# Kernel optimization log

Hardware: AMD Instinct MI355X
Metric: run time of the kernel (lower is better)

## Reference

```python
import jax, jax.numpy as jnp
import numpy as np

DIM = 768
HEADS = 8
HEAD_DIM = DIM // HEADS
K_TOP = 10
NUM_ANSWERS = 128000
BATCH = 1024
LN_EPS = 1e-5
NORM_EPS = 1e-12


def setup_inputs() -> dict:
    key = jax.random.key(0)
    ks = jax.random.split(key, 16)
    s = 0.02  # weight init scale
    return {
        "visual_feat": jax.random.normal(ks[0], (BATCH, DIM), jnp.float32),
        "text_feat": jax.random.normal(ks[1], (BATCH, DIM), jnp.float32),
        "candidate_mask": (jax.random.uniform(ks[2], (BATCH, NUM_ANSWERS), jnp.float32) > 0.5).astype(jnp.float32),
        "answer_embeddings": jax.random.normal(ks[3], (NUM_ANSWERS, DIM), jnp.float32),
        # MultiheadAttention params (torch layout: y = x @ W.T + b)
        "wq": jax.random.normal(ks[4], (DIM, DIM), jnp.float32) * s,
        "bq": jnp.zeros((DIM,), jnp.float32),
        "wk": jax.random.normal(ks[5], (DIM, DIM), jnp.float32) * s,
        "bk": jnp.zeros((DIM,), jnp.float32),
        "wv": jax.random.normal(ks[6], (DIM, DIM), jnp.float32) * s,
        "bv": jnp.zeros((DIM,), jnp.float32),
        "wo": jax.random.normal(ks[7], (DIM, DIM), jnp.float32) * s,
        "bo": jnp.zeros((DIM,), jnp.float32),
        # fusion_proj: Linear(2*dim -> dim) + LayerNorm(dim)
        "fusion_w": jax.random.normal(ks[8], (DIM, 2 * DIM), jnp.float32) * s,
        "fusion_b": jnp.zeros((DIM,), jnp.float32),
        "ln_g": jnp.ones((DIM,), jnp.float32),
        "ln_b": jnp.zeros((DIM,), jnp.float32),
        # similarity_proj: Linear(dim -> dim)
        "sim_w": jax.random.normal(ks[9], (DIM, DIM), jnp.float32) * s,
        "sim_b": jnp.zeros((DIM,), jnp.float32),
    }


def _l2norm(x):
    # F.normalize: x / clamp_min(||x||, eps)
    n = jnp.sqrt(jnp.sum(x * x, axis=-1, keepdims=True))
    return x / jnp.maximum(n, NORM_EPS)


def _forward(visual_feat, text_feat, candidate_mask, answer_embeddings,
             wq, bq, wk, bk, wv, bv, wo, bo,
             fusion_w, fusion_b, ln_g, ln_b, sim_w, sim_b):
    B = visual_feat.shape[0]
    # Multihead attention with q=text (len 1), k=v=visual (len 1).
    q = text_feat @ wq.T + bq            # [B, D]
    k = visual_feat @ wk.T + bk          # [B, D]
    v = visual_feat @ wv.T + bv          # [B, D]
    qh = q.reshape(B, HEADS, HEAD_DIM)
    kh = k.reshape(B, HEADS, HEAD_DIM)
    vh = v.reshape(B, HEADS, HEAD_DIM)
    scores = jnp.sum(qh * kh, axis=-1) / jnp.sqrt(jnp.float32(HEAD_DIM))  # [B, H]
    # softmax over the single key position -> identically 1
    attn_w = jax.nn.softmax(scores[..., None], axis=-1)                   # [B, H, 1]
    attended = (attn_w * vh).reshape(B, DIM) @ wo.T + bo                  # [B, D]
    # fusion_proj: Linear -> LayerNorm -> GELU (dropout is identity in eval)
    fused_in = jnp.concatenate([visual_feat, attended], axis=-1)          # [B, 2D]
    h = fused_in @ fusion_w.T + fusion_b                                  # [B, D]
    mu = jnp.mean(h, axis=-1, keepdims=True)
    var = jnp.mean((h - mu) ** 2, axis=-1, keepdims=True)
    h = (h - mu) / jnp.sqrt(var + LN_EPS) * ln_g + ln_b
    fused = jax.nn.gelu(h, approximate=False)
    fused_proj = fused @ sim_w.T + sim_b                                  # [B, D]
    # normalize + similarity GEMM + mask + top-k + gather
    similarity = _l2norm(fused_proj) @ _l2norm(answer_embeddings).T       # [B, A]
    similarity = similarity * candidate_mask
    topk_scores, topk_indices = jax.lax.top_k(similarity, K_TOP)          # [B, K]
    topk_embeddings = answer_embeddings[topk_indices]                     # [B, K, D]
    return topk_scores, topk_indices, topk_embeddings


def reference(visual_feat, text_feat, candidate_mask, answer_embeddings,
              wq, bq, wk, bk, wv, bv, wo, bo,
              fusion_w, fusion_b, ln_g, ln_b, sim_w, sim_b):
    return _forward(visual_feat, text_feat, candidate_mask, answer_embeddings,
                    wq, bq, wk, bk, wv, bv, wo, bo,
                    fusion_w, fusion_b, ln_g, ln_b, sim_w, sim_b)
```

## Files before the change

kernel.cpp:

```cpp
#include <hip/hip_runtime.h>
#include <math.h>

#define DIM    768
#define BATCH  1024
#define NANS   128000
#define NT128  1000
#define NWORDS 4000

typedef short  bf16x8 __attribute__((ext_vector_type(8)));
typedef float  f32x4  __attribute__((ext_vector_type(4)));
typedef unsigned long long u64;

__device__ __forceinline__ short f2bf(float x)
{
    unsigned u = __builtin_bit_cast(unsigned, x);
    u += 0x7fffu + ((u >> 16) & 1u);
    return (short)(u >> 16);
}

__device__ __forceinline__ void gload16(const void* g, void* l)
{
    __builtin_amdgcn_global_load_lds(
        (const __attribute__((address_space(1))) void*)g,
        (__attribute__((address_space(3))) void*)l, 16, 0, 0);
}

__device__ __forceinline__ unsigned f2sort(float s)
{
    unsigned u = __builtin_bit_cast(unsigned, s);
    return u ^ ((unsigned)((int)u >> 31) | 0x80000000u);
}

__device__ __forceinline__ unsigned umaxu(unsigned a, unsigned b) { return a > b ? a : b; }
__device__ __forceinline__ unsigned uminu(unsigned a, unsigned b) { return a < b ? a : b; }

struct Top10k { unsigned k0,k1,k2,k3,k4,k5,k6,k7,k8,k9; };
__device__ __forceinline__ void t10k_init(Top10k& t)
{ t.k0=t.k1=t.k2=t.k3=t.k4=t.k5=t.k6=t.k7=t.k8=t.k9=0u; }
__device__ __forceinline__ void t10k_ins(Top10k& t, unsigned v)
{
#define TS(K) { unsigned mx = umaxu(v, t.K); v = uminu(v, t.K); t.K = mx; }
    TS(k0) TS(k1) TS(k2) TS(k3) TS(k4) TS(k5) TS(k6) TS(k7) TS(k8) TS(k9)
#undef TS
}

struct Top16u { u64 k0,k1,k2,k3,k4,k5,k6,k7,k8,k9,k10,k11,k12,k13,k14,k15; };
__device__ __forceinline__ void t16u_init(Top16u& t)
{
    t.k0=t.k1=t.k2=t.k3=t.k4=t.k5=t.k6=t.k7=0ull;
    t.k8=t.k9=t.k10=t.k11=t.k12=t.k13=t.k14=t.k15=0ull;
}
__device__ __forceinline__ void t16u_ins(Top16u& t, u64 v)
{
#define TS(K) { bool g = v > t.K; u64 mx = g ? v : t.K; v = g ? t.K : v; t.K = mx; }
    TS(k0)  TS(k1)  TS(k2)  TS(k3)  TS(k4)  TS(k5)  TS(k6)  TS(k7)
    TS(k8)  TS(k9)  TS(k10) TS(k11) TS(k12) TS(k13) TS(k14) TS(k15)
#undef TS
}

__global__ __launch_bounds__(256, 2) void gemm_bias_k(
    const float* __restrict__ A, int lda,
    const float* __restrict__ W,
    const float* __restrict__ bias,
    float* __restrict__ C, int ldc, int K)
{
    __shared__ float as[32][68];
    __shared__ float bs[32][68];
    int m0 = blockIdx.x * 64, n0 = blockIdx.y * 64;
    int tid = threadIdx.x;
    int tm = tid & 15, tn = tid >> 4;
    int sr = tid >> 3, skq = tid & 7;
    float acc[4][4] = {};
    for (int k0 = 0; k0 < K; k0 += 32) {
        __syncthreads();
        #pragma unroll
        for (int p = 0; p < 2; ++p) {
            int r = sr + 32 * p;
            float4 av = *(const float4*)&A[(size_t)(m0 + r) * lda + k0 + skq * 4];
            as[skq*4+0][r] = av.x; as[skq*4+1][r] = av.y;
            as[skq*4+2][r] = av.z; as[skq*4+3][r] = av.w;
            float4 wv = *(const float4*)&W[(size_t)(n0 + r) * K + k0 + skq * 4];
            bs[skq*4+0][r] = wv.x; bs[skq*4+1][r] = wv.y;
            bs[skq*4+2][r] = wv.z; bs[skq*4+3][r] = wv.w;
        }
        __syncthreads();
        #pragma unroll 8
        for (int k = 0; k < 32; ++k) {
            float a4[4], b4[4];
            *(float4*)a4 = *(const float4*)&as[k][tm*4];
            *(float4*)b4 = *(const float4*)&bs[k][tn*4];
            #pragma unroll
            for (int i = 0; i < 4; ++i)
                #pragma unroll
                for (int j = 0; j < 4; ++j)
                    acc[i][j] = fmaf(a4[i], b4[j], acc[i][j]);
        }
    }
    float4 bv4 = *(const float4*)&bias[n0 + tn*4];
    #pragma unroll
    for (int i = 0; i < 4; ++i) {
        float4 c4;
        c4.x = acc[i][0] + bv4.x; c4.y = acc[i][1] + bv4.y;
        c4.z = acc[i][2] + bv4.z; c4.w = acc[i][3] + bv4.w;
        *(float4*)&C[(size_t)(m0 + tm*4 + i) * ldc + n0 + tn*4] = c4;
    }
}

__global__ void copy_visual_k(const float* __restrict__ src, float* __restrict__ dst)
{
    int idx = blockIdx.x * 256 + threadIdx.x;
    const int total = BATCH * (DIM / 4);
    for (; idx < total; idx += 512 * 256) {
        int b = idx / (DIM / 4), c = idx % (DIM / 4);
        ((float4*)dst)[(size_t)b * (1536 / 4) + c] = ((const float4*)src)[idx];
    }
}

__device__ __forceinline__ float block_sum(float v, float* red)
{
    #pragma unroll
    for (int o = 32; o; o >>= 1) v += __shfl_down(v, o);
    if ((threadIdx.x & 63) == 0) red[threadIdx.x >> 6] = v;
    __syncthreads();
    float r = red[0] + red[1] + red[2] + red[3];
    __syncthreads();
    return r;
}

__global__ __launch_bounds__(256) void ln_gelu_k(float* __restrict__ H,
        const float* __restrict__ g, const float* __restrict__ b)
{
    __shared__ float red[4];
    int row = blockIdx.x, tid = threadIdx.x;
    float* hr = H + (size_t)row * DIM;
    float v0 = hr[tid], v1 = hr[tid + 256], v2 = hr[tid + 512];
    float mu = block_sum(v0 + v1 + v2, red) * (1.0f / 768.0f);
    float d0 = v0 - mu, d1 = v1 - mu, d2 = v2 - mu;
    float var = block_sum(d0*d0 + d1*d1 + d2*d2, red) * (1.0f / 768.0f);
    float rinv = 1.0f / sqrtf(var + 1e-5f);
    #pragma unroll
    for (int q = 0; q < 3; ++q) {
        int d = tid + 256 * q;
        float dd = (q == 0 ? d0 : (q == 1 ? d1 : d2));
        float y = dd * rinv * g[d] + b[d];
        hr[d] = 0.5f * y * (1.0f + erff(y * 0.70710678118654752f));
    }
}

__global__ __launch_bounds__(256) void l2norm_bf_k(float* __restrict__ P,
        short* __restrict__ Pb)
{
    __shared__ float red[4];
    int row = blockIdx.x, tid = threadIdx.x;
    float* pr = P + (size_t)row * DIM;
    short* pb = Pb + (size_t)row * DIM;
    float v0 = pr[tid], v1 = pr[tid + 256], v2 = pr[tid + 512];
    float ss = block_sum(v0*v0 + v1*v1 + v2*v2, red);
    float inv = 1.0f / fmaxf(sqrtf(ss), 1e-12f);
    v0 *= inv; v1 *= inv; v2 *= inv;
    pr[tid] = v0; pr[tid + 256] = v1; pr[tid + 512] = v2;
    pb[tid] = f2bf(v0); pb[tid + 256] = f2bf(v1); pb[tid + 512] = f2bf(v2);
}

__global__ __launch_bounds__(256) void prep_ans_k(
    const float* __restrict__ ANS, int row0, int nrows,
    double* __restrict__ inv64, short* __restrict__ AB)
{
    int r = blockIdx.x * 4 + (threadIdx.x >> 6);
    if (r >= nrows) return;
    int row = row0 + r;
    int lane = threadIdx.x & 63;
    const float4* a4 = (const float4*)(ANS + (size_t)row * DIM);
    float4 x0 = a4[lane], x1 = a4[lane + 64], x2 = a4[lane + 128];
    double ss = (double)x0.x*x0.x + (double)x0.y*x0.y + (double)x0.z*x0.z + (double)x0.w*x0.w
              + (double)x1.x*x1.x + (double)x1.y*x1.y + (double)x1.z*x1.z + (double)x1.w*x1.w
              + (double)x2.x*x2.x + (double)x2.y*x2.y + (double)x2.z*x2.z + (double)x2.w*x2.w;
    #pragma unroll
    for (int o = 32; o; o >>= 1) ss += __shfl_xor(ss, o);
    double inv = 1.0 / fmax(sqrt(ss), 1e-12);
    if (lane == 0) inv64[row] = inv;
    float invf = (float)inv;
    short* ob = AB + (size_t)r * DIM;
    ushort4 o0, o1, o2;
    o0.x = (unsigned short)f2bf(x0.x*invf); o0.y = (unsigned short)f2bf(x0.y*invf);
    o0.z = (unsigned short)f2bf(x0.z*invf); o0.w = (unsigned short)f2bf(x0.w*invf);
    o1.x = (unsigned short)f2bf(x1.x*invf); o1.y = (unsigned short)f2bf(x1.y*invf);
    o1.z = (unsigned short)f2bf(x1.z*invf); o1.w = (unsigned short)f2bf(x1.w*invf);
    o2.x = (unsigned short)f2bf(x2.x*invf); o2.y = (unsigned short)f2bf(x2.y*invf);
    o2.z = (unsigned short)f2bf(x2.z*invf); o2.w = (unsigned short)f2bf(x2.w*invf);
    *(ushort4*)&ob[lane * 4]           = o0;
    *(ushort4*)&ob[(lane + 64) * 4]    = o1;
    *(ushort4*)&ob[(lane + 128) * 4]   = o2;
}

__global__ __launch_bounds__(256, 4) void prep_maskT_k(
    const float* __restrict__ mask, unsigned* __restrict__ bitsT)
{
    int r = blockIdx.x * 256 + threadIdx.x;
    int w0 = blockIdx.y * 40;
    const float* mr = mask + (size_t)r * NANS;
    for (int w = w0; w < w0 + 40; ++w) {
        const float4* p = (const float4*)(mr + w * 32);
        unsigned b = 0;
        #pragma unroll
        for (int q = 0; q < 8; ++q) {
            float4 v = p[q];
            b |= ((unsigned)(v.x != 0.f)) << (q*4+0);
            b |= ((unsigned)(v.y != 0.f)) << (q*4+1);
            b |= ((unsigned)(v.z != 0.f)) << (q*4+2);
            b |= ((unsigned)(v.w != 0.f)) << (q*4+3);
        }
        bitsT[(size_t)w * BATCH + r] = b;
    }
}

__global__ __launch_bounds__(256, 2) void gemmsel_k(
    const short* __restrict__ Pb,
    const short* __restrict__ AB,
    const unsigned* __restrict__ bitsT,
    unsigned* __restrict__ ck,
    int t128_0, int nt128)
{
    __shared__ __align__(16) char smem[33792];
    float* scl = (float*)smem;

    int bid = blockIdx.x;
    int v = (bid & 7) * nt128 + (bid >> 3);
    int at = v >> 3, bt = v & 7;
    int gt = t128_0 + at;
    int a0l = at * 128, b0 = bt * 128;

    int tid = threadIdx.x;
    int lane = tid & 63, wid = tid >> 6;
    int wm = wid & 1, wn = wid >> 1;
    int lr = lane & 15, lg = lane >> 4;

    const char* gA0 = (const char*)(AB + (size_t)(a0l + (tid >> 2)) * DIM + (tid & 3) * 8);
    const char* gA1 = (const char*)(AB + (size_t)(a0l + 64 + (tid >> 2)) * DIM + (tid & 3) * 8);
    const char* gB0 = (const char*)(Pb + (size_t)(b0 + (tid >> 2)) * DIM + (tid & 3) * 8);
    const char* gB1 = (const char*)(Pb + (size_t)(b0 + 64 + (tid >> 2)) * DIM + (tid & 3) * 8);

    f32x4 acc[4][4];
    #pragma unroll
    for (int i = 0; i < 4; ++i)
        #pragma unroll
        for (int j = 0; j < 4; ++j)
            acc[i][j] = (f32x4){0.f, 0.f, 0.f, 0.f};

    {
        char* la = smem + tid * 16;
        gload16(gA0, la);
        gload16(gA1, la + 4096);
        gload16(gB0, la + 16384);
        gload16(gB1, la + 20480);
    }
    __syncthreads();

    int buf = 0;
    for (int kt = 0; kt < 24; ++kt) {
        if (kt < 23) {
            int kb = (kt + 1) * 64;
            char* la = smem + (buf ^ 1) * 8192 + tid * 16;
            gload16(gA0 + kb, la);
            gload16(gA1 + kb, la + 4096);
            gload16(gB0 + kb, la + 16384);
            gload16(gB1 + kb, la + 20480);
        }
        const short* a_sh = (const short*)(smem + buf * 8192);
        const short* b_sh = (const short*)(smem + 16384 + buf * 8192);
        bf16x8 af[4], bg[4];
        #pragma unroll
        for (int mt = 0; mt < 4; ++mt)
            af[mt] = *(const bf16x8*)(a_sh + (wm*64 + mt*16 + lr) * 32 + lg*8);
        #pragma unroll
        for (int nt = 0; nt < 4; ++nt)
            bg[nt] = *(const bf16x8*)(b_sh + (wn*64 + nt*16 + lr) * 32 + lg*8);
        #pragma unroll
        for (int mt = 0; mt < 4; ++mt)
            #pragma unroll
            for (int nt = 0; nt < 4; ++nt)
                acc[mt][nt] = __builtin_amdgcn_mfma_f32_16x16x32_bf16(
                    af[mt], bg[nt], acc[mt][nt], 0, 0, 0);
        __syncthreads();
        buf ^= 1;
    }

    Top10k tp;
    t10k_init(tp);
    int col = tid >> 1, qt = tid & 1;
    int qoff = qt * 32;

    for (int c = 0; c < 2; ++c) {
        __syncthreads();
        if (wm == c) {
            #pragma unroll
            for (int nt = 0; nt < 4; ++nt) {
                int lcol = wn * 64 + nt * 16 + lr;
                #pragma unroll
                for (int mt = 0; mt < 4; ++mt) {
                    int lrow = mt * 16 + lg * 4;
                    scl[(lrow + 0) * 132 + lcol] = acc[mt][nt][0];
                    scl[(lrow + 1) * 132 + lcol] = acc[mt][nt][1];
                    scl[(lrow + 2) * 132 + lcol] = acc[mt][nt][2];
                    scl[(lrow + 3) * 132 + lcol] = acc[mt][nt][3];
                }
            }
        }
        __syncthreads();
        unsigned wv = bitsT[(size_t)(gt * 4 + c * 2 + qt) * BATCH + b0 + col];
        unsigned lobc = (unsigned)(127 - c * 64 - qoff);
        #pragma unroll
        for (int i = 0; i < 32; ++i) {
            float sc = scl[(qoff + i) * 132 + col];
            sc = ((wv >> i) & 1u) ? sc : 0.0f;
            unsigned key = (f2sort(sc) & 0xFFFFFF80u) | (lobc - (unsigned)i);
            t10k_ins(tp, key);
        }
    }

    unsigned q0 = __shfl_xor(tp.k0, 1), q1 = __shfl_xor(tp.k1, 1);
    unsigned q2 = __shfl_xor(tp.k2, 1), q3 = __shfl_xor(tp.k3, 1);
    unsigned q4 = __shfl_xor(tp.k4, 1), q5 = __shfl_xor(tp.k5, 1);
    unsigned q6 = __shfl_xor(tp.k6, 1), q7 = __shfl_xor(tp.k7, 1);
    unsigned q8 = __shfl_xor(tp.k8, 1), q9 = __shfl_xor(tp.k9, 1);
    if (qt == 0) {
        unsigned* dst = ck + (size_t)(b0 + col) * (NT128 * 10) + (size_t)gt * 10;
        dst[0] = umaxu(tp.k0, q9);
        dst[1] = umaxu(tp.k1, q8);
        dst[2] = umaxu(tp.k2, q7);
        dst[3] = umaxu(tp.k3, q6);
        dst[4] = umaxu(tp.k4, q5);
        dst[5] = umaxu(tp.k5, q4);
        dst[6] = umaxu(tp.k6, q3);
        dst[7] = umaxu(tp.k7, q2);
        dst[8] = umaxu(tp.k8, q1);
        dst[9] = umaxu(tp.k9, q0);
    }
}

__global__ __launch_bounds__(256) void merge_rescore5_k(
    const unsigned* __restrict__ ck,
    const float* __restrict__ P, const float* __restrict__ ANS,
    const double* __restrict__ invn64, const float* __restrict__ mask,
    float* __restrict__ out)
{
    __shared__ u64    lk[4096];
    __shared__ u64    rrk[4];
    __shared__ int    rrp[4];
    __shared__ int    topi_s[16];
    __shared__ double tops_s[16];
    __shared__ int    fin_s[10];
    int row = blockIdx.x, tid = threadIdx.x;

    Top16u t;
    t16u_init(t);
    const unsigned* ckr = ck + (size_t)row * (NT128 * 10);
    for (int j = tid; j < NT128 * 10; j += 256)
        t16u_ins(t, ((u64)ckr[j] << 32) | (unsigned)j);
    {
        int o = tid * 16;
        lk[o+0]=t.k0;  lk[o+1]=t.k1;  lk[o+2]=t.k2;  lk[o+3]=t.k3;
        lk[o+4]=t.k4;  lk[o+5]=t.k5;  lk[o+6]=t.k6;  lk[o+7]=t.k7;
        lk[o+8]=t.k8;  lk[o+9]=t.k9;  lk[o+10]=t.k10; lk[o+11]=t.k11;
        lk[o+12]=t.k12; lk[o+13]=t.k13; lk[o+14]=t.k14; lk[o+15]=t.k15;
    }
    __syncthreads();

    for (int it = 0; it < 16; ++it) {
        u64 bk = 0; int bp = -1;
        for (int j = tid; j < 4096; j += 256) {
            u64 k = lk[j];
            if (k > bk) { bk = k; bp = j; }
        }
        #pragma unroll
        for (int o = 32; o; o >>= 1) {
            u64 ok = __shfl_down(bk, o);
            int op = __shfl_down(bp, o);
            if (ok > bk) { bk = ok; bp = op; }
        }
        if ((tid & 63) == 0) { rrk[tid >> 6] = bk; rrp[tid >> 6] = bp; }
        __syncthreads();
        if (tid == 0) {
            for (int w = 1; w < 4; ++w)
                if (rrk[w] > bk) { bk = rrk[w]; bp = rrp[w]; }
            unsigned key = (unsigned)(bk >> 32);
            int pos = (int)(bk & 0xffffffffull);
            topi_s[it] = (pos / 10) * 128 + 127 - (int)(key & 0x7Fu);
            lk[bp] = 0;
        }
        __syncthreads();
    }

    int c = tid >> 4, part = tid & 15;
    int aidx = topi_s[c];
    const float4* p4 = (const float4*)(P + (size_t)row * DIM);
    const float4* a4 = (const float4*)(ANS + (size_t)aidx * DIM);
    double sum = 0.0;
    #pragma unroll
    for (int i = 0; i < 12; ++i) {
        float4 pv = p4[part * 12 + i];
        float4 av = a4[part * 12 + i];
        sum += (double)pv.x * av.x + (double)pv.y * av.y
             + (double)pv.z * av.z + (double)pv.w * av.w;
    }
    #pragma unroll
    for (int o = 8; o; o >>= 1) sum += __shfl_down(sum, o, 16);
    if (part == 0) {
        float m = mask[(size_t)row * NANS + aidx];
        tops_s[c] = sum * invn64[aidx] * (double)m;
    }
    __syncthreads();

    if (tid == 0) {
        unsigned used = 0;
        for (int k = 0; k < 10; ++k) {
            int bj = -1;
            for (int j = 0; j < 16; ++j) {
                if (used & (1u << j)) continue;
                if (bj < 0 || tops_s[j] > tops_s[bj] ||
                    (tops_s[j] == tops_s[bj] && topi_s[j] < topi_s[bj])) bj = j;
            }
            used |= 1u << bj;
            out[(size_t)row * 10 + k] = (float)tops_s[bj];
            out[10240 + (size_t)row * 10 + k] = (float)topi_s[bj];
            fin_s[k] = topi_s[bj];
        }
    }
    __syncthreads();

    for (int k = 0; k < 10; ++k) {
        int id = fin_s[k];
        const float* arow = ANS + (size_t)id * DIM;
        float* orow = out + 20480 + ((size_t)(row * 10 + k)) * DIM;
        for (int d = tid; d < DIM; d += 256) orow[d] = arow[d];
    }
}

extern "C" void kernel_launch(void* const* d_in, const int* in_sizes, int n_in,
                              void* d_out, int out_size, void* d_ws, size_t ws_size,
                              hipStream_t stream)
{
    (void)in_sizes; (void)n_in; (void)out_size;
    const float* visual = (const float*)d_in[0];
    const float* mask   = (const float*)d_in[2];
    const float* ans    = (const float*)d_in[3];
    const float* wv = (const float*)d_in[8];
    const float* bv = (const float*)d_in[9];
    const float* wo = (const float*)d_in[10];
    const float* bo = (const float*)d_in[11];
    const float* fw = (const float*)d_in[12];
    const float* fb = (const float*)d_in[13];
    const float* lg = (const float*)d_in[14];
    const float* lb = (const float*)d_in[15];
    const float* sw = (const float*)d_in[16];
    const float* sb = (const float*)d_in[17];
    float* out = (float*)d_out;

    char* w = (char*)d_ws;
    float*    P      = (float*)w;    w += (size_t)BATCH * DIM * 4;
    short*    Pb     = (short*)w;    w += (size_t)BATCH * DIM * 2;
    double*   invn64 = (double*)w;   w += (size_t)NANS * 8;
    unsigned* ck     = (unsigned*)w; w += (size_t)BATCH * NT128 * 10 * 4;
    unsigned* bitsT  = (unsigned*)w; w += (size_t)NWORDS * BATCH * 4;
    char*     tail   = w;
    float*    fused_in = (float*)tail;
    float*    v        = fused_in + (size_t)BATCH * 1536;
    float*    h        = v + (size_t)BATCH * DIM;
    short*    AB       = (short*)tail;

    size_t ab_t = (size_t)128 * DIM * 2;
    size_t used = (size_t)(tail - (char*)d_ws);
    size_t avail = (ws_size > used) ? (ws_size - used) : ab_t;
    int CT = (int)(avail / ab_t);
    if (CT < 1) CT = 1;
    if (CT > NT128) CT = NT128;
    int nch = (NT128 + CT - 1) / CT;

    copy_visual_k<<<512, 256, 0, stream>>>(visual, fused_in);
    gemm_bias_k<<<dim3(16, 12), 256, 0, stream>>>(visual, DIM, wv, bv, v, DIM, DIM);
    gemm_bias_k<<<dim3(16, 12), 256, 0, stream>>>(v, DIM, wo, bo, fused_in + DIM, 1536, DIM);
    gemm_bias_k<<<dim3(16, 12), 256, 0, stream>>>(fused_in, 1536, fw, fb, h, DIM, 1536);
    ln_gelu_k<<<BATCH, 256, 0, stream>>>(h, lg, lb);
    gemm_bias_k<<<dim3(16, 12), 256, 0, stream>>>(h, DIM, sw, sb, P, DIM, DIM);
    l2norm_bf_k<<<BATCH, 256, 0, stream>>>(P, Pb);
    prep_maskT_k<<<dim3(4, 100), 256, 0, stream>>>(mask, bitsT);

    for (int ch = 0; ch < nch; ++ch) {
        int t0 = ch * CT;
        int n = NT128 - t0; if (n > CT) n = CT;
        int nrows = n * 128;
        prep_ans_k<<<(nrows + 3) / 4, 256, 0, stream>>>(ans, t0 * 128, nrows,
                                                        invn64, AB);
        gemmsel_k<<<n * 8, 256, 0, stream>>>(Pb, AB, bitsT, ck, t0, n);
    }

    merge_rescore5_k<<<BATCH, 256, 0, stream>>>(ck, P, ans, invn64, mask, out);
}
```

Measured before the change: 965.8 us.

## Split fusion GEMM to drop concat copy, retile mask prep, transpose score staging

The concat copy of visual features is removed. The fusion projection is computed as two K=768 GEMMs, the second one accumulating into the output, with a weight-stride parameter added to gemm_bias_k. The mask bit-packing kernel launches twice as many blocks, each handling half as many words, to raise parallelism on the large mask read. The score staging in gemmsel is transposed to a column-major layout so each thread writes and reads float4 vectors instead of scalars. Together these aim to cut copies, LDS instruction count and mask-prep latency, at the cost of one extra GEMM launch and a read-modify-write pass over the fusion output.

```diff
diff --git a/kernel.cpp b/kernel.cpp
--- a/kernel.cpp
+++ b/kernel.cpp
@@ -60,9 +60,9 @@
 
 __global__ __launch_bounds__(256, 2) void gemm_bias_k(
     const float* __restrict__ A, int lda,
-    const float* __restrict__ W,
+    const float* __restrict__ W, int wstride,
     const float* __restrict__ bias,
-    float* __restrict__ C, int ldc, int K)
+    float* __restrict__ C, int ldc, int K, int accum)
 {
     __shared__ float as[32][68];
     __shared__ float bs[32][68];
@@ -79,7 +79,7 @@
             float4 av = *(const float4*)&A[(size_t)(m0 + r) * lda + k0 + skq * 4];
             as[skq*4+0][r] = av.x; as[skq*4+1][r] = av.y;
             as[skq*4+2][r] = av.z; as[skq*4+3][r] = av.w;
-            float4 wv = *(const float4*)&W[(size_t)(n0 + r) * K + k0 + skq * 4];
+            float4 wv = *(const float4*)&W[(size_t)(n0 + r) * wstride + k0 + skq * 4];
             bs[skq*4+0][r] = wv.x; bs[skq*4+1][r] = wv.y;
             bs[skq*4+2][r] = wv.z; bs[skq*4+3][r] = wv.w;
         }
@@ -96,23 +96,24 @@
                     acc[i][j] = fmaf(a4[i], b4[j], acc[i][j]);
         }
     }
-    float4 bv4 = *(const float4*)&bias[n0 + tn*4];
-    #pragma unroll
-    for (int i = 0; i < 4; ++i) {
-        float4 c4;
-        c4.x = acc[i][0] + bv4.x; c4.y = acc[i][1] + bv4.y;
-        c4.z = acc[i][2] + bv4.z; c4.w = acc[i][3] + bv4.w;
-        *(float4*)&C[(size_t)(m0 + tm*4 + i) * ldc + n0 + tn*4] = c4;
-    }
-}
-
-__global__ void copy_visual_k(const float* __restrict__ src, float* __restrict__ dst)
-{
-    int idx = blockIdx.x * 256 + threadIdx.x;
-    const int total = BATCH * (DIM / 4);
-    for (; idx < total; idx += 512 * 256) {
-        int b = idx / (DIM / 4), c = idx % (DIM / 4);
-        ((float4*)dst)[(size_t)b * (1536 / 4) + c] = ((const float4*)src)[idx];
+    if (accum) {
+        #pragma unroll
+        for (int i = 0; i < 4; ++i) {
+            float* cp = &C[(size_t)(m0 + tm*4 + i) * ldc + n0 + tn*4];
+            float4 c4 = *(float4*)cp;
+            c4.x += acc[i][0]; c4.y += acc[i][1];
+            c4.z += acc[i][2]; c4.w += acc[i][3];
+            *(float4*)cp = c4;
+        }
+    } else {
+        float4 bv4 = *(const float4*)&bias[n0 + tn*4];
+        #pragma unroll
+        for (int i = 0; i < 4; ++i) {
+            float4 c4;
+            c4.x = acc[i][0] + bv4.x; c4.y = acc[i][1] + bv4.y;
+            c4.z = acc[i][2] + bv4.z; c4.w = acc[i][3] + bv4.w;
+            *(float4*)&C[(size_t)(m0 + tm*4 + i) * ldc + n0 + tn*4] = c4;
+        }
     }
 }
 
@@ -197,9 +198,9 @@
     const float* __restrict__ mask, unsigned* __restrict__ bitsT)
 {
     int r = blockIdx.x * 256 + threadIdx.x;
-    int w0 = blockIdx.y * 40;
+    int w0 = blockIdx.y * 20;
     const float* mr = mask + (size_t)r * NANS;
-    for (int w = w0; w < w0 + 40; ++w) {
+    for (int w = w0; w < w0 + 20; ++w) {
         const float4* p = (const float4*)(mr + w * 32);
         unsigned b = 0;
         #pragma unroll
@@ -221,7 +222,7 @@
     unsigned* __restrict__ ck,
     int t128_0, int nt128)
 {
-    __shared__ __align__(16) char smem[33792];
+    __shared__ __align__(16) char smem[34816];
     float* scl = (float*)smem;
 
     int bid = blockIdx.x;
@@ -299,10 +300,7 @@
                 #pragma unroll
                 for (int mt = 0; mt < 4; ++mt) {
                     int lrow = mt * 16 + lg * 4;
-                    scl[(lrow + 0) * 132 + lcol] = acc[mt][nt][0];
-                    scl[(lrow + 1) * 132 + lcol] = acc[mt][nt][1];
-                    scl[(lrow + 2) * 132 + lcol] = acc[mt][nt][2];
-                    scl[(lrow + 3) * 132 + lcol] = acc[mt][nt][3];
+                    *(f32x4*)&scl[lcol * 68 + lrow] = acc[mt][nt];
                 }
             }
         }
@@ -310,11 +308,15 @@
         unsigned wv = bitsT[(size_t)(gt * 4 + c * 2 + qt) * BATCH + b0 + col];
         unsigned lobc = (unsigned)(127 - c * 64 - qoff);
         #pragma unroll
-        for (int i = 0; i < 32; ++i) {
-            float sc = scl[(qoff + i) * 132 + col];
-            sc = ((wv >> i) & 1u) ? sc : 0.0f;
-            unsigned key = (f2sort(sc) & 0xFFFFFF80u) | (lobc - (unsigned)i);
-            t10k_ins(tp, key);
+        for (int i4 = 0; i4 < 8; ++i4) {
+            f32x4 s4 = *(const f32x4*)&scl[col * 68 + qoff + i4 * 4];
+            #pragma unroll
+            for (int j = 0; j < 4; ++j) {
+                int i = i4 * 4 + j;
+                float sc = ((wv >> i) & 1u) ? s4[j] : 0.0f;
+                unsigned key = (f2sort(sc) & 0xFFFFFF80u) | (lobc - (unsigned)i);
+                t10k_ins(tp, key);
+            }
         }
     }
 
@@ -463,10 +465,10 @@
     unsigned* ck     = (unsigned*)w; w += (size_t)BATCH * NT128 * 10 * 4;
     unsigned* bitsT  = (unsigned*)w; w += (size_t)NWORDS * BATCH * 4;
     char*     tail   = w;
-    float*    fused_in = (float*)tail;
-    float*    v        = fused_in + (size_t)BATCH * 1536;
-    float*    h        = v + (size_t)BATCH * DIM;
-    short*    AB       = (short*)tail;
+    float*    v      = (float*)tail;
+    float*    att    = v + (size_t)BATCH * DIM;
+    float*    h      = att + (size_t)BATCH * DIM;
+    short*    AB     = (short*)tail;
 
     size_t ab_t = (size_t)128 * DIM * 2;
     size_t used = (size_t)(tail - (char*)d_ws);
@@ -476,14 +478,14 @@
     if (CT > NT128) CT = NT128;
     int nch = (NT128 + CT - 1) / CT;
 
-    copy_visual_k<<<512, 256, 0, stream>>>(visual, fused_in);
-    gemm_bias_k<<<dim3(16, 12), 256, 0, stream>>>(visual, DIM, wv, bv, v, DIM, DIM);
-    gemm_bias_k<<<dim3(16, 12), 256, 0, stream>>>(v, DIM, wo, bo, fused_in + DIM, 1536, DIM);
-    gemm_bias_k<<<dim3(16, 12), 256, 0, stream>>>(fused_in, 1536, fw, fb, h, DIM, 1536);
+    gemm_bias_k<<<dim3(16, 12), 256, 0, stream>>>(visual, DIM, wv, DIM, bv, v, DIM, DIM, 0);
+    gemm_bias_k<<<dim3(16, 12), 256, 0, stream>>>(v, DIM, wo, DIM, bo, att, DIM, DIM, 0);
+    gemm_bias_k<<<dim3(16, 12), 256, 0, stream>>>(visual, DIM, fw, 2*DIM, fb, h, DIM, DIM, 0);
+    gemm_bias_k<<<dim3(16, 12), 256, 0, stream>>>(att, DIM, fw + DIM, 2*DIM, nullptr, h, DIM, DIM, 1);
     ln_gelu_k<<<BATCH, 256, 0, stream>>>(h, lg, lb);
-    gemm_bias_k<<<dim3(16, 12), 256, 0, stream>>>(h, DIM, sw, sb, P, DIM, DIM);
+    gemm_bias_k<<<dim3(16, 12), 256, 0, stream>>>(h, DIM, sw, DIM, sb, P, DIM, DIM, 0);
     l2norm_bf_k<<<BATCH, 256, 0, stream>>>(P, Pb);
-    prep_maskT_k<<<dim3(4, 100), 256, 0, stream>>>(mask, bitsT);
+    prep_maskT_k<<<dim3(4, 200), 256, 0, stream>>>(mask, bitsT);
 
     for (int ch = 0; ch < nch; ++ch) {
         int t0 = ch * CT;
```

After: 1.002 ms. 3.8% more time.
